# Optimization experiments

Hardware: AMD Instinct MI355X
Metric: run time of the kernel (lower is better)

## Reference

```python
import jax, jax.numpy as jnp
import numpy as np

EPS = 1e-6


def setup_inputs() -> dict:
    key = jax.random.key(0)
    ks = jax.random.split(key, 8)
    B, L, C = 2, 512, 768  # d_model=768, C//3=256
    pairDim = 128
    inp = {
        "x": jax.random.normal(ks[0], (B, L, C), dtype=jnp.float32),
        "ln_w": jnp.ones((C,), jnp.float32),
        "ln_b": jnp.zeros((C,), jnp.float32),
        # torch Linear weights are [out, in]
        "W1": jax.random.normal(ks[1], (256, C // 3), jnp.float32) * (1.0 / np.sqrt(C // 3)),
        "b1": jax.random.normal(ks[2], (256,), jnp.float32) * 0.02,
        "Wa": jax.random.normal(ks[3], (64, 64), jnp.float32) * (1.0 / np.sqrt(64)),
        "ba": jax.random.normal(ks[4], (64,), jnp.float32) * 0.02,
        "W2": jax.random.normal(ks[5], (pairDim, 32), jnp.float32) * (1.0 / np.sqrt(32)),
        "b2": jax.random.normal(ks[6], (pairDim,), jnp.float32) * 0.02,
    }
    return inp


def _layernorm(x, w, b):
    mu = jnp.mean(x, axis=-1, keepdims=True)
    var = jnp.mean(jnp.square(x - mu), axis=-1, keepdims=True)
    return (x - mu) * jax.lax.rsqrt(var + EPS) * w + b


def reference(x, ln_w, ln_b, W1, b1, Wa, ba, W2, b2):
    B, L, C = x.shape
    h = _layernorm(x, ln_w, ln_b)                      # [B,L,C]
    h = h.reshape(B, L, 3, C // 3)                     # [B,L,3,C/3]
    t = (h @ W1.T + b1).reshape(B, L, 3, 32, 8)        # [B,L,3,32,8]
    # outer product t[...,i]*t[...,j] then mean over the 3 chunks (fused)
    mean_out = jnp.einsum('blkci,blkcj->blcij', t, t) / 3.0  # [B,L,32,8,8]
    mean_out = mean_out.reshape(B, L, 32, 64).transpose(0, 2, 1, 3)  # [B,32,L,64]
    mean_trans = jax.nn.gelu(mean_out @ Wa.T + ba, approximate=False)  # [B,32,L,64]
    raw = jnp.einsum('bcld,bcmd->bclm', mean_out, mean_trans)  # [B,32,L,L]
    raw = raw.transpose(0, 2, 3, 1)                    # [B,L,L,32]
    return raw @ W2.T + b2                             # [B,L,L,pairDim]
```

## Files before the change

### kernel.cpp

```cpp
#include <hip/hip_runtime.h>
#include <math.h>


typedef __attribute__((ext_vector_type(8))) _Float16 half8;
typedef __attribute__((ext_vector_type(4))) _Float16 half4;
typedef __attribute__((ext_vector_type(4))) float f32x4;

#define MFMA_F16(a,b,c) __builtin_amdgcn_mfma_f32_16x16x32_f16((a),(b),(c),0,0,0)

static __device__ inline unsigned pack2f16(float a, float b) {
    _Float16 ha = (_Float16)a, hb = (_Float16)b;
    unsigned short ua = __builtin_bit_cast(unsigned short, ha);
    unsigned short ub = __builtin_bit_cast(unsigned short, hb);
    return (unsigned)ua | ((unsigned)ub << 16);
}

static __device__ inline half8 cvt8(float4 u, float4 v) {
    half8 h;
    h[0] = (_Float16)u.x; h[1] = (_Float16)u.y; h[2] = (_Float16)u.z; h[3] = (_Float16)u.w;
    h[4] = (_Float16)v.x; h[5] = (_Float16)v.y; h[6] = (_Float16)v.z; h[7] = (_Float16)v.w;
    return h;
}

__global__ __launch_bounds__(256) void k0_pack(const float* __restrict__ W1, _Float16* __restrict__ W1H)
{
    int flat8 = blockIdx.x * 256 + threadIdx.x;
    int j  = flat8 >> 5, i8 = flat8 & 31;
    int nt = j >> 4, lr = j & 15, ks = i8 >> 2, lk = i8 & 3;
    const float4* src = (const float4*)(W1 + (size_t)j * 256 + (size_t)i8 * 8);
    half8 h = cvt8(src[0], src[1]);
    *(half8*)(W1H + (((size_t)(nt * 8 + ks) * 64) + lk * 16 + lr) * 8) = h;
}

__global__ __launch_bounds__(256) void k1_rowstage2(
    const float* __restrict__ x, const float* __restrict__ ln_w, const float* __restrict__ ln_b,
    const _Float16* __restrict__ W1H, const float* __restrict__ b1,
    const float* __restrict__ Wa, const float* __restrict__ ba,
    _Float16* __restrict__ mo_g, _Float16* __restrict__ mt_g)
{
    const int blk = blockIdx.x;
    const int b   = blk >> 8;
    const int l0  = (blk & 255) << 1;
    const int tid = threadIdx.x;
    const int w   = tid >> 6;
    const int lane = tid & 63;
    const int lr  = lane & 15;
    const int lk  = lane >> 4;

    __shared__ _Float16 hs16[16 * 280];
    __shared__ float ts2[2][776];
    __shared__ float mos2[2][2176];

    half8 waf[2];
    #pragma unroll
    for (int ks = 0; ks < 2; ++ks) {
        const float* wp = Wa + (size_t)(w * 16 + lr) * 64 + ks * 32 + lk * 8;
        waf[ks] = cvt8(*(const float4*)wp, *(const float4*)(wp + 4));
    }
    const float4 baq = *(const float4*)(ba + w * 16 + lk * 4);

    if (w < 2) {
        const float4* xrow = (const float4*)(x + ((size_t)(b * 512 + l0 + w)) * 768);
        float4 xv[3];
        float s1 = 0.f, s2 = 0.f;
        #pragma unroll
        for (int e4 = 0; e4 < 3; ++e4) {
            float4 v = xrow[lane + 64 * e4];
            xv[e4] = v;
            s1 += v.x + v.y + v.z + v.w;
            s2 += v.x * v.x + v.y * v.y + v.z * v.z + v.w * v.w;
        }
        #pragma unroll
        for (int off = 32; off > 0; off >>= 1) {
            s1 += __shfl_xor(s1, off);
            s2 += __shfl_xor(s2, off);
        }
        float mu   = s1 * (1.0f / 768.0f);
        float var  = s2 * (1.0f / 768.0f) - mu * mu;
        float rstd = rsqrtf(var + 1e-6f);
        #pragma unroll
        for (int e4 = 0; e4 < 3; ++e4) {
            float4 lw = ((const float4*)ln_w)[lane + 64 * e4];
            float4 lb = ((const float4*)ln_b)[lane + 64 * e4];
            half4 h4;
            h4[0] = (_Float16)((xv[e4].x - mu) * rstd * lw.x + lb.x);
            h4[1] = (_Float16)((xv[e4].y - mu) * rstd * lw.y + lb.y);
            h4[2] = (_Float16)((xv[e4].z - mu) * rstd * lw.z + lb.z);
            h4[3] = (_Float16)((xv[e4].w - mu) * rstd * lw.w + lb.w);
            *(half4*)&hs16[(w * 3 + e4) * 280 + 4 * lane] = h4;
        }
    }
    __syncthreads();

    {
        f32x4 acc[4] = {};
        #pragma unroll
        for (int ks = 0; ks < 8; ++ks) {
            half8 af = *(const half8*)&hs16[lr * 280 + ks * 32 + lk * 8];
            #pragma unroll
            for (int n = 0; n < 4; ++n) {
                half8 bf = *(const half8*)(W1H + (((size_t)((w * 4 + n) * 8 + ks) * 64) + lane) * 8);
                acc[n] = MFMA_F16(af, bf, acc[n]);
            }
        }
        #pragma unroll
        for (int n = 0; n < 4; ++n) {
            int j = (w * 4 + n) * 16 + lr;
            float bb = b1[j];
            #pragma unroll
            for (int jj = 0; jj < 4; ++jj) {
                int m = lk * 4 + jj;
                if (m < 6) {
                    int r = (m >= 3) ? 1 : 0, k = m - r * 3;
                    ts2[r][k * 256 + j] = acc[n][jj] + bb;
                }
            }
        }
    }
    __syncthreads();

    {
        const int c = tid >> 3, i = tid & 7;
        #pragma unroll
        for (int r = 0; r < 2; ++r) {
            float ti0 = ts2[r][c * 8 + i], ti1 = ts2[r][256 + c * 8 + i], ti2 = ts2[r][512 + c * 8 + i];
            half8 h8;
            #pragma unroll
            for (int j = 0; j < 8; j++) {
                float m = (ti0 * ts2[r][c * 8 + j] + ti1 * ts2[r][256 + c * 8 + j]
                         + ti2 * ts2[r][512 + c * 8 + j]) * (1.0f / 3.0f);
                mos2[r][c * 68 + i * 8 + j] = m;
                h8[j] = (_Float16)m;
            }
            size_t mobase = ((size_t)(b * 32 + c) * 512 + (l0 + r)) * 64 + i * 8;
            *(half8*)(mo_g + mobase) = h8;
        }
    }
    __syncthreads();

    #pragma unroll
    for (int nt2 = 0; nt2 < 4; ++nt2) {
        const int r = nt2 >> 1, ch = nt2 & 1;
        f32x4 acc = { baq.x, baq.y, baq.z, baq.w };
        #pragma unroll
        for (int ks = 0; ks < 2; ++ks) {
            const float* mp = &mos2[r][(ch * 16 + lr) * 68 + ks * 32 + lk * 8];
            half8 mof = cvt8(*(const float4*)mp, *(const float4*)(mp + 4));
            acc = MFMA_F16(waf[ks], mof, acc);
        }
        half4 o;
        #pragma unroll
        for (int j = 0; j < 4; ++j) {
            float g = 0.5f * acc[j] * (1.0f + erff(acc[j] * 0.70710678118654752f));
            o[j] = (_Float16)g;
        }
        *(half4*)(mt_g + ((size_t)(b * 32 + ch * 16 + lr) * 512 + (l0 + r)) * 64 + w * 16 + lk * 4) = o;
    }
}

__global__ __launch_bounds__(256, 2) void k2_mfma(
    const _Float16* __restrict__ mo, const _Float16* __restrict__ mt,
    const float* __restrict__ W2, const float* __restrict__ b2,
    float* __restrict__ out)
{
    __shared__ _Float16 raw16[512 * 40];
    __shared__ float sc[4][2048];

    const int tid  = threadIdx.x;
    const int w    = tid >> 6;
    const int lane = tid & 63;
    const int lr   = lane & 15;
    const int lk   = lane >> 4;

    const int flat = blockIdx.x;
    const int nf   = (flat & 7) * 128 + (flat >> 3);
    const int m0   = (nf & 31) << 4;
    const int l0   = ((nf >> 5) & 15) << 5;
    const int b    = nf >> 9;

    #pragma unroll
    for (int cp = 0; cp < 4; ++cp) {
        const int c0 = w * 8 + cp * 2;
        f32x4 acc[2][2] = {};
        #pragma unroll
        for (int ci = 0; ci < 2; ++ci) {
            const int c = c0 + ci;
            const _Float16* mo_c = mo + (((size_t)(b * 32 + c) * 512) + l0) * 64;
            const _Float16* mt_c = mt + (((size_t)(b * 32 + c) * 512) + m0) * 64;
            #pragma unroll
            for (int ks = 0; ks < 2; ++ks) {
                half8 bfrag = *(const half8*)(mt_c + (size_t)lr * 64 + ks * 32 + lk * 8);
                #pragma unroll
                for (int rh = 0; rh < 2; ++rh) {
                    half8 afrag = *(const half8*)(mo_c + (size_t)(rh * 16 + lr) * 64 + ks * 32 + lk * 8);
                    acc[ci][rh] = MFMA_F16(afrag, bfrag, acc[ci][rh]);
                }
            }
        }
        #pragma unroll
        for (int rh = 0; rh < 2; ++rh) {
            #pragma unroll
            for (int j = 0; j < 4; ++j) {
                int pair = (rh * 16 + lk * 4 + j) * 16 + lr;
                int sw   = (((pair >> 3) & 1) << 3) | (((pair >> 6) & 1) << 4);
                *(unsigned*)&raw16[pair * 40 + (c0 ^ sw)] = pack2f16(acc[0][rh][j], acc[1][rh][j]);
            }
        }
    }

    half8 wfrag[8]; float4 b2q[8];
    #pragma unroll
    for (int c8 = 0; c8 < 8; ++c8) {
        const float* wp = W2 + (size_t)(c8 * 16 + lr) * 32 + lk * 8;
        wfrag[c8] = cvt8(*(const float4*)wp, *(const float4*)(wp + 4));
        b2q[c8]   = *(const float4*)(b2 + c8 * 16 + lk * 4);
    }
    __syncthreads();

    for (int i = 0; i < 8; ++i) {
        const int r  = w * 8 + i;
        const int pr = r * 16 + lr;
        const int swr = (((pr >> 3) & 1) << 3) | (((pr >> 6) & 1) << 4);
        half8 a = *(const half8*)&raw16[pr * 40 + ((lk * 8) ^ swr)];

        #pragma unroll
        for (int c8 = 0; c8 < 8; ++c8) {
            f32x4 d = { b2q[c8].x, b2q[c8].y, b2q[c8].z, b2q[c8].w };
            d = MFMA_F16(wfrag[c8], a, d);
            int chunk = (c8 * 4 + lk) ^ lr;
            *(f32x4*)&sc[w][lr * 128 + chunk * 4] = d;
        }
        float* ob = out + (((size_t)(b * 512 + l0 + r)) * 512 + m0) * 128;
        #pragma unroll
        for (int s = 0; s < 8; ++s) {
            int mm = s * 2 + (lane >> 5);
            int cp = (lane & 31) ^ mm;
            f32x4 v = *(const f32x4*)&sc[w][mm * 128 + cp * 4];
            __builtin_nontemporal_store(v, (f32x4*)(ob + s * 256 + lane * 4));
        }
    }
}

extern "C" void kernel_launch(void* const* d_in, const int* in_sizes, int n_in,
                              void* d_out, int out_size, void* d_ws, size_t ws_size,
                              hipStream_t stream) {
    const float* x    = (const float*)d_in[0];
    const float* ln_w = (const float*)d_in[1];
    const float* ln_b = (const float*)d_in[2];
    const float* W1   = (const float*)d_in[3];
    const float* b1   = (const float*)d_in[4];
    const float* Wa   = (const float*)d_in[5];
    const float* ba   = (const float*)d_in[6];
    const float* W2   = (const float*)d_in[7];
    const float* b2   = (const float*)d_in[8];
    float* out = (float*)d_out;

    _Float16* mo  = (_Float16*)d_ws;
    _Float16* mt  = mo + (size_t)2 * 32 * 512 * 64;
    _Float16* W1H = mt + (size_t)2 * 32 * 512 * 64;

    k0_pack<<<32, 256, 0, stream>>>(W1, W1H);
    k1_rowstage2<<<512, 256, 0, stream>>>(x, ln_w, ln_b, W1H, b1, Wa, ba, mo, mt);
    k2_mfma<<<1024, 256, 0, stream>>>(mo, mt, W2, b2, out);
}
```

Baseline: 76.29 us.

## Enlarge k2 tile to 32x32 pairs and alias the output staging onto raw16

The k2 kernel now computes a 32x32 (l,m) tile per block instead of 32x16, halving the grid to 512 blocks. Each A fragment of mo is reused against two mt fragments. The first-stage results are preloaded into registers, which lets the per-wave output staging buffer reuse the raw16 shared memory. The aim is fewer redundant global loads per output and better amortised setup, at the cost of more registers, a doubled raw16 buffer and fewer blocks for occupancy and tail balance.

```diff
diff --git a/kernel.cpp b/kernel.cpp
--- a/kernel.cpp
+++ b/kernel.cpp
@@ -158,13 +158,12 @@
     }
 }
 
-__global__ __launch_bounds__(256, 2) void k2_mfma(
+__global__ __launch_bounds__(256, 2) void k2_mfma32(
     const _Float16* __restrict__ mo, const _Float16* __restrict__ mt,
     const float* __restrict__ W2, const float* __restrict__ b2,
     float* __restrict__ out)
 {
-    __shared__ _Float16 raw16[512 * 40];
-    __shared__ float sc[4][2048];
+    __shared__ _Float16 raw16[1024 * 40];
 
     const int tid  = threadIdx.x;
     const int w    = tid >> 6;
@@ -173,15 +172,15 @@
     const int lk   = lane >> 4;
 
     const int flat = blockIdx.x;
-    const int nf   = (flat & 7) * 128 + (flat >> 3);
-    const int m0   = (nf & 31) << 4;
-    const int l0   = ((nf >> 5) & 15) << 5;
-    const int b    = nf >> 9;
+    const int nf   = (flat & 7) * 64 + (flat >> 3);
+    const int m0   = (nf & 15) << 5;
+    const int l0   = ((nf >> 4) & 15) << 5;
+    const int b    = nf >> 8;
 
     #pragma unroll
     for (int cp = 0; cp < 4; ++cp) {
         const int c0 = w * 8 + cp * 2;
-        f32x4 acc[2][2] = {};
+        f32x4 acc[2][2][2] = {};
         #pragma unroll
         for (int ci = 0; ci < 2; ++ci) {
             const int c = c0 + ci;
@@ -189,22 +188,25 @@
             const _Float16* mt_c = mt + (((size_t)(b * 32 + c) * 512) + m0) * 64;
             #pragma unroll
             for (int ks = 0; ks < 2; ++ks) {
-                half8 bfrag = *(const half8*)(mt_c + (size_t)lr * 64 + ks * 32 + lk * 8);
+                half8 bfr0 = *(const half8*)(mt_c + (size_t)lr * 64 + ks * 32 + lk * 8);
+                half8 bfr1 = *(const half8*)(mt_c + (size_t)(16 + lr) * 64 + ks * 32 + lk * 8);
                 #pragma unroll
                 for (int rh = 0; rh < 2; ++rh) {
-                    half8 afrag = *(const half8*)(mo_c + (size_t)(rh * 16 + lr) * 64 + ks * 32 + lk * 8);
-                    acc[ci][rh] = MFMA_F16(afrag, bfrag, acc[ci][rh]);
+                    half8 af = *(const half8*)(mo_c + (size_t)(rh * 16 + lr) * 64 + ks * 32 + lk * 8);
+                    acc[ci][rh][0] = MFMA_F16(af, bfr0, acc[ci][rh][0]);
+                    acc[ci][rh][1] = MFMA_F16(af, bfr1, acc[ci][rh][1]);
                 }
             }
         }
         #pragma unroll
-        for (int rh = 0; rh < 2; ++rh) {
-            #pragma unroll
-            for (int j = 0; j < 4; ++j) {
-                int pair = (rh * 16 + lk * 4 + j) * 16 + lr;
-                int sw   = (((pair >> 3) & 1) << 3) | (((pair >> 6) & 1) << 4);
-                *(unsigned*)&raw16[pair * 40 + (c0 ^ sw)] = pack2f16(acc[0][rh][j], acc[1][rh][j]);
-            }
+        for (int rh = 0; rh < 2; ++rh)
+        #pragma unroll
+        for (int mh = 0; mh < 2; ++mh)
+        #pragma unroll
+        for (int j = 0; j < 4; ++j) {
+            int pair = (rh * 16 + lk * 4 + j) * 32 + mh * 16 + lr;
+            int sw   = (((pair >> 3) & 1) << 3) | (((pair >> 7) & 1) << 4);
+            *(unsigned*)&raw16[pair * 40 + (c0 ^ sw)] = pack2f16(acc[0][rh][mh][j], acc[1][rh][mh][j]);
         }
     }
 
@@ -217,26 +219,39 @@
     }
     __syncthreads();
 
+    half8 afr[8][2];
+    #pragma unroll
+    for (int i = 0; i < 8; ++i)
+    #pragma unroll
+    for (int mh = 0; mh < 2; ++mh) {
+        int pr = (w * 8 + i) * 32 + mh * 16 + lr;
+        int sw = (((pr >> 3) & 1) << 3) | (((pr >> 7) & 1) << 4);
+        afr[i][mh] = *(const half8*)&raw16[pr * 40 + ((lk * 8) ^ sw)];
+    }
+    float* scw = (float*)&raw16[(size_t)w * 256 * 40];
+
+    #pragma unroll
     for (int i = 0; i < 8; ++i) {
-        const int r  = w * 8 + i;
-        const int pr = r * 16 + lr;
-        const int swr = (((pr >> 3) & 1) << 3) | (((pr >> 6) & 1) << 4);
-        half8 a = *(const half8*)&raw16[pr * 40 + ((lk * 8) ^ swr)];
-
-        #pragma unroll
-        for (int c8 = 0; c8 < 8; ++c8) {
-            f32x4 d = { b2q[c8].x, b2q[c8].y, b2q[c8].z, b2q[c8].w };
-            d = MFMA_F16(wfrag[c8], a, d);
-            int chunk = (c8 * 4 + lk) ^ lr;
-            *(f32x4*)&sc[w][lr * 128 + chunk * 4] = d;
+        const int r = w * 8 + i;
+        #pragma unroll
+        for (int mh = 0; mh < 2; ++mh) {
+            const int m = mh * 16 + lr;
+            #pragma unroll
+            for (int c8 = 0; c8 < 8; ++c8) {
+                f32x4 d = { b2q[c8].x, b2q[c8].y, b2q[c8].z, b2q[c8].w };
+                d = MFMA_F16(wfrag[c8], afr[i][mh], d);
+                int chunk = (c8 * 4 + lk) ^ m;
+                *(f32x4*)&scw[m * 128 + chunk * 4] = d;
+            }
         }
         float* ob = out + (((size_t)(b * 512 + l0 + r)) * 512 + m0) * 128;
         #pragma unroll
-        for (int s = 0; s < 8; ++s) {
-            int mm = s * 2 + (lane >> 5);
-            int cp = (lane & 31) ^ mm;
-            f32x4 v = *(const f32x4*)&sc[w][mm * 128 + cp * 4];
-            __builtin_nontemporal_store(v, (f32x4*)(ob + s * 256 + lane * 4));
+        for (int s = 0; s < 16; ++s) {
+            int flatq = s * 256 + lane * 4;
+            int m = flatq >> 7;
+            int cpos = (flatq >> 2) & 31;
+            f32x4 v = *(const f32x4*)&scw[m * 128 + ((cpos ^ m) * 4)];
+            __builtin_nontemporal_store(v, (f32x4*)(ob + flatq));
         }
     }
 }
@@ -261,5 +276,5 @@
 
     k0_pack<<<32, 256, 0, stream>>>(W1, W1H);
     k1_rowstage2<<<512, 256, 0, stream>>>(x, ln_w, ln_b, W1H, b1, Wa, ba, mo, mt);
-    k2_mfma<<<1024, 256, 0, stream>>>(mo, mt, W2, b2, out);
-}
+    k2_mfma32<<<512, 256, 0, stream>>>(mo, mt, W2, b2, out);
+}
```

Result: slower. 81.23 us (+6.5%).

## Split row-stage kernel into LN+GEMM1 and outer-product+GEMM2 kernels

Applied to the files above, without the earlier changes.

Splits the fused row-stage kernel into two launches. The first does layernorm and the first linear layer and writes the projected rows to a float workspace. The second runs one row per block for the outer-product mean and the Wa GEMM with GELU. This gives smaller shared-memory footprints and more blocks for the second stage. In exchange it adds an extra kernel launch and a global round trip for the intermediate tensor.

```diff
diff --git a/kernel.cpp b/kernel.cpp
--- a/kernel.cpp
+++ b/kernel.cpp
@@ -32,11 +32,10 @@
     *(half8*)(W1H + (((size_t)(nt * 8 + ks) * 64) + lk * 16 + lr) * 8) = h;
 }
 
-__global__ __launch_bounds__(256) void k1_rowstage2(
+__global__ __launch_bounds__(256) void k1a_ln_gemm1(
     const float* __restrict__ x, const float* __restrict__ ln_w, const float* __restrict__ ln_b,
     const _Float16* __restrict__ W1H, const float* __restrict__ b1,
-    const float* __restrict__ Wa, const float* __restrict__ ba,
-    _Float16* __restrict__ mo_g, _Float16* __restrict__ mt_g)
+    float* __restrict__ tg)
 {
     const int blk = blockIdx.x;
     const int b   = blk >> 8;
@@ -49,15 +48,6 @@
 
     __shared__ _Float16 hs16[16 * 280];
     __shared__ float ts2[2][776];
-    __shared__ float mos2[2][2176];
-
-    half8 waf[2];
-    #pragma unroll
-    for (int ks = 0; ks < 2; ++ks) {
-        const float* wp = Wa + (size_t)(w * 16 + lr) * 64 + ks * 32 + lk * 8;
-        waf[ks] = cvt8(*(const float4*)wp, *(const float4*)(wp + 4));
-    }
-    const float4 baq = *(const float4*)(ba + w * 16 + lk * 4);
 
     if (w < 2) {
         const float4* xrow = (const float4*)(x + ((size_t)(b * 512 + l0 + w)) * 768);
@@ -119,32 +109,69 @@
     }
     __syncthreads();
 
+    #pragma unroll
+    for (int rep = 0; rep < 2; ++rep) {
+        int idx4 = tid + rep * 256;
+        if (idx4 < 384) {
+            int r = idx4 / 192, o4 = idx4 - r * 192;
+            float4 v = *(const float4*)&ts2[r][o4 * 4];
+            *(float4*)(tg + ((size_t)(b * 512 + l0 + r)) * 768 + o4 * 4) = v;
+        }
+    }
+}
+
+__global__ __launch_bounds__(256) void k1b_outer_gemm2(
+    const float* __restrict__ tg, const float* __restrict__ Wa, const float* __restrict__ ba,
+    _Float16* __restrict__ mo_g, _Float16* __restrict__ mt_g)
+{
+    const int blk = blockIdx.x;
+    const int b   = blk >> 9;
+    const int l   = blk & 511;
+    const int tid = threadIdx.x;
+    const int w   = tid >> 6;
+    const int lane = tid & 63;
+    const int lr  = lane & 15;
+    const int lk  = lane >> 4;
+
+    __shared__ float ts[776];
+    __shared__ float mos[32 * 68];
+
+    half8 waf[2];
+    #pragma unroll
+    for (int ks = 0; ks < 2; ++ks) {
+        const float* wp = Wa + (size_t)(w * 16 + lr) * 64 + ks * 32 + lk * 8;
+        waf[ks] = cvt8(*(const float4*)wp, *(const float4*)(wp + 4));
+    }
+    const float4 baq = *(const float4*)(ba + w * 16 + lk * 4);
+
+    if (tid < 192) {
+        float4 v = ((const float4*)(tg + (size_t)(b * 512 + l) * 768))[tid];
+        *(float4*)&ts[tid * 4] = v;
+    }
+    __syncthreads();
+
     {
         const int c = tid >> 3, i = tid & 7;
-        #pragma unroll
-        for (int r = 0; r < 2; ++r) {
-            float ti0 = ts2[r][c * 8 + i], ti1 = ts2[r][256 + c * 8 + i], ti2 = ts2[r][512 + c * 8 + i];
-            half8 h8;
-            #pragma unroll
-            for (int j = 0; j < 8; j++) {
-                float m = (ti0 * ts2[r][c * 8 + j] + ti1 * ts2[r][256 + c * 8 + j]
-                         + ti2 * ts2[r][512 + c * 8 + j]) * (1.0f / 3.0f);
-                mos2[r][c * 68 + i * 8 + j] = m;
-                h8[j] = (_Float16)m;
-            }
-            size_t mobase = ((size_t)(b * 32 + c) * 512 + (l0 + r)) * 64 + i * 8;
-            *(half8*)(mo_g + mobase) = h8;
-        }
-    }
-    __syncthreads();
-
-    #pragma unroll
-    for (int nt2 = 0; nt2 < 4; ++nt2) {
-        const int r = nt2 >> 1, ch = nt2 & 1;
+        float ti0 = ts[c * 8 + i], ti1 = ts[256 + c * 8 + i], ti2 = ts[512 + c * 8 + i];
+        half8 h8;
+        #pragma unroll
+        for (int j = 0; j < 8; j++) {
+            float m = (ti0 * ts[c * 8 + j] + ti1 * ts[256 + c * 8 + j]
+                     + ti2 * ts[512 + c * 8 + j]) * (1.0f / 3.0f);
+            mos[c * 68 + i * 8 + j] = m;
+            h8[j] = (_Float16)m;
+        }
+        size_t mobase = ((size_t)(b * 32 + c) * 512 + l) * 64 + i * 8;
+        *(half8*)(mo_g + mobase) = h8;
+    }
+    __syncthreads();
+
+    #pragma unroll
+    for (int ch = 0; ch < 2; ++ch) {
         f32x4 acc = { baq.x, baq.y, baq.z, baq.w };
         #pragma unroll
         for (int ks = 0; ks < 2; ++ks) {
-            const float* mp = &mos2[r][(ch * 16 + lr) * 68 + ks * 32 + lk * 8];
+            const float* mp = &mos[(ch * 16 + lr) * 68 + ks * 32 + lk * 8];
             half8 mof = cvt8(*(const float4*)mp, *(const float4*)(mp + 4));
             acc = MFMA_F16(waf[ks], mof, acc);
         }
@@ -154,7 +181,7 @@
             float g = 0.5f * acc[j] * (1.0f + erff(acc[j] * 0.70710678118654752f));
             o[j] = (_Float16)g;
         }
-        *(half4*)(mt_g + ((size_t)(b * 32 + ch * 16 + lr) * 512 + (l0 + r)) * 64 + w * 16 + lk * 4) = o;
+        *(half4*)(mt_g + ((size_t)(b * 32 + ch * 16 + lr) * 512 + l) * 64 + w * 16 + lk * 4) = o;
     }
 }
 
@@ -258,8 +285,10 @@
     _Float16* mo  = (_Float16*)d_ws;
     _Float16* mt  = mo + (size_t)2 * 32 * 512 * 64;
     _Float16* W1H = mt + (size_t)2 * 32 * 512 * 64;
+    float* tg     = (float*)(W1H + 65536);
 
     k0_pack<<<32, 256, 0, stream>>>(W1, W1H);
-    k1_rowstage2<<<512, 256, 0, stream>>>(x, ln_w, ln_b, W1H, b1, Wa, ba, mo, mt);
+    k1a_ln_gemm1<<<512, 256, 0, stream>>>(x, ln_w, ln_b, W1H, b1, tg);
+    k1b_outer_gemm2<<<1024, 256, 0, stream>>>(tg, Wa, ba, mo, mt);
     k2_mfma<<<1024, 256, 0, stream>>>(mo, mt, W2, b2, out);
 }
```

New measurement: 80.68 us. 1.06x slower.
